# Optimization experiments

Measured on AMD Instinct MI355X. Metric: run time of the kernel, lower is better.

Reference implementation:

```python
import jax, jax.numpy as jnp
import numpy as np

T = 4096        # tokens
D = 1024        # input_dim
H = 2048        # expert_hidden_dim
O = 1024        # output_dim
E = 8           # num_experts
K = 2           # top_k


def setup_inputs() -> dict:
    key = jax.random.key(0)
    ks = jax.random.split(key, 7)
    s_in = 1.0 / np.sqrt(D)
    s_h = 1.0 / np.sqrt(H)
    return {
        "x": jax.random.normal(ks[0], (T, D), dtype=jnp.float32),
        "Wg": jax.random.uniform(ks[1], (D, E), jnp.float32, -s_in, s_in),
        "bg": jax.random.uniform(ks[2], (E,), jnp.float32, -s_in, s_in),
        "W1": jax.random.uniform(ks[3], (E, D, H), jnp.float32, -s_in, s_in),
        "b1": jax.random.uniform(ks[4], (E, H), jnp.float32, -s_in, s_in),
        "W2": jax.random.uniform(ks[5], (E, H, O), jnp.float32, -s_h, s_h),
        "b2": jax.random.uniform(ks[6], (E, O), jnp.float32, -s_h, s_h),
    }


def reference(x, Wg, bg, W1, b1, W2, b2):
    # Gating: top-k over expert logits, softmax over the k selected logits.
    logits = x @ Wg + bg                                  # [T, E]
    top_vals, top_idx = jax.lax.top_k(logits, K)          # [T, K]
    gates = jax.nn.softmax(top_vals, axis=-1)             # [T, K]

    # Expert MLPs (Linear -> ReLU -> Linear). Each token is processed by the
    # experts it routes to; since an expert's output on x is route-independent,
    # compute all expert outputs once and gather the selected ones (static
    # shapes, jit-friendly equivalent of the masked dispatch loop).
    h = jax.nn.relu(jnp.einsum('td,edh->eth', x, W1) + b1[:, None, :])  # [E,T,H]
    y = jnp.einsum('eth,eho->eto', h, W2) + b2[:, None, :]              # [E,T,O]

    sel = y[top_idx, jnp.arange(T)[:, None]]              # [T, K, O]
    # Weighted combine (scatter_add over batch_idx == per-token sum over K).
    return jnp.sum(sel * gates[..., None], axis=1)        # [T, O]
```

## Files before the change

### kernel.cpp

```cpp
#include <hip/hip_runtime.h>
#include <math.h>


#define T_TOK 4096
#define DIM   1024
#define HID   2048
#define OUTD  1024
#define NE    8

typedef __bf16 bf16_t;
typedef __bf16 bf16x8 __attribute__((ext_vector_type(8)));
typedef float  f32x4  __attribute__((ext_vector_type(4)));

typedef __attribute__((address_space(3))) void       as3_void;
typedef __attribute__((address_space(1))) const void as1_void;
#define GLDS16(src, dst) \
  __builtin_amdgcn_global_load_lds((as1_void*)(src), (as3_void*)(dst), 16, 0, 0)

#define FENCE() asm volatile("" ::: "memory")
#define BARRIER() do { FENCE(); __builtin_amdgcn_s_barrier(); FENCE(); } while (0)
#define LGKM_WAIT() do { \
    asm volatile("s_waitcnt lgkmcnt(0)" ::: "memory"); \
    __builtin_amdgcn_sched_barrier(0); } while (0)
#define VMW_RING() do { \
    if (wid < 4) asm volatile("s_waitcnt vmcnt(4)" ::: "memory"); \
    else         asm volatile("s_waitcnt vmcnt(3)" ::: "memory"); } while (0)
#define VM_WAIT0() asm volatile("s_waitcnt vmcnt(0)" ::: "memory")

__global__ void k_gate(const float* __restrict__ x, const float* __restrict__ Wg,
                       const float* __restrict__ bg, int* __restrict__ einfo,
                       float2* __restrict__ gpair, bf16_t* __restrict__ xb) {
  int wid  = threadIdx.x >> 6;
  int lane = threadIdx.x & 63;
  int t = blockIdx.x * 4 + wid;

  const float4* xr = (const float4*)(x + (size_t)t * DIM);
  float4 xv4[4];
  float sf[NE];
#pragma unroll
  for (int e = 0; e < NE; ++e) sf[e] = 0.f;

#pragma unroll
  for (int i = 0; i < 4; ++i) {
    int q = lane + 64 * i;
    float4 xv = xr[q];
    xv4[i] = xv;
    int d = q * 4;
#pragma unroll
    for (int c = 0; c < 4; ++c) {
      float xc = (&xv.x)[c];
      const float4* wr = (const float4*)(Wg + (size_t)(d + c) * NE);
      float4 w0 = wr[0], w1 = wr[1];
      sf[0] += xc * w0.x; sf[1] += xc * w0.y;
      sf[2] += xc * w0.z; sf[3] += xc * w0.w;
      sf[4] += xc * w1.x; sf[5] += xc * w1.y;
      sf[6] += xc * w1.z; sf[7] += xc * w1.w;
    }
  }

  ushort4* xbr = (ushort4*)(xb + (size_t)t * DIM);
#pragma unroll
  for (int i = 0; i < 4; ++i) {
    union { bf16_t b[4]; ushort4 u; } cv;
    cv.b[0] = (bf16_t)xv4[i].x; cv.b[1] = (bf16_t)xv4[i].y;
    cv.b[2] = (bf16_t)xv4[i].z; cv.b[3] = (bf16_t)xv4[i].w;
    xbr[lane + 64 * i] = cv.u;
  }

  double s[NE];
#pragma unroll
  for (int e = 0; e < NE; ++e) s[e] = (double)sf[e];
#pragma unroll
  for (int off = 32; off > 0; off >>= 1) {
#pragma unroll
    for (int e = 0; e < NE; ++e) s[e] += __shfl_xor(s[e], off);
  }

  if (lane == 0) {
    double v0 = -1e300, v1 = -1e300;
    int i0 = 0, i1 = 0;
#pragma unroll
    for (int e = 0; e < NE; ++e) {
      double v = s[e] + (double)bg[e];
      if (v > v0)      { v1 = v0; i1 = i0; v0 = v; i0 = e; }
      else if (v > v1) { v1 = v;  i1 = e; }
    }
    float ex = expf((float)(v1 - v0));
    float inv = 1.0f / (1.0f + ex);
    einfo[t] = i0 | (i1 << 8);
    gpair[t] = make_float2(inv, ex * inv);
  }
}

__global__ void k_bin(const int* __restrict__ einfo, const float2* __restrict__ gpair,
                      int* __restrict__ cnt, int* __restrict__ offs,
                      int* __restrict__ elist, float* __restrict__ egate,
                      int* __restrict__ tokrec) {
  __shared__ int scnt[NE];
  int w = threadIdx.x >> 6;
  int lane = threadIdx.x & 63;
  unsigned long long below = (lane == 0) ? 0ull : ((~0ull) >> (64 - lane));
  int base = 0;
  for (int c = 0; c < T_TOK / 64; ++c) {
    int t = c * 64 + lane;
    int ei = einfo[t];
    float2 g = gpair[t];
    int e0 = ei & 0xff, e1 = ei >> 8;
    bool m0 = (e0 == w);
    bool m  = m0 || (e1 == w);
    unsigned long long mask = __ballot(m);
    if (m) {
      int pos = base + (int)__popcll(mask & below);
      elist[w * T_TOK + pos] = t;
      egate[w * T_TOK + pos] = m0 ? g.x : g.y;
      tokrec[2 * t + (m0 ? 0 : 1)] = (w << 16) | pos;
    }
    base += (int)__popcll(mask);
  }
  if (lane == 0) scnt[w] = base;
  __syncthreads();
  if (threadIdx.x == 0) {
    int a = 0;
#pragma unroll
    for (int e = 0; e < NE; ++e) {
      cnt[e] = scnt[e];
      offs[e] = a;
      a += scnt[e];
    }
    offs[NE] = a;
  }
}

__global__ void k_tr(const float* __restrict__ W, bf16_t* __restrict__ Wt,
                     int R, int C) {
  __shared__ float tile[64][68];
  size_t ebase = (size_t)blockIdx.z * R * C;
  int c0 = blockIdx.x * 64, r0 = blockIdx.y * 64;
  int tid = threadIdx.x;
  int ty = tid >> 4, tx = tid & 15;
#pragma unroll
  for (int i = 0; i < 4; ++i) {
    int row = ty + i * 16;
    float4 v = *(const float4*)&W[ebase + (size_t)(r0 + row) * C + c0 + tx * 4];
    *(float4*)&tile[row][tx * 4] = v;
  }
  __syncthreads();
  int oc = tid >> 2, seg = tid & 3;
#pragma unroll
  for (int half = 0; half < 2; ++half) {
    union { bf16_t b[8]; uint4 u; } cv;
#pragma unroll
    for (int r = 0; r < 8; ++r)
      cv.b[r] = (bf16_t)tile[seg * 16 + half * 8 + r][oc];
    *(uint4*)&Wt[ebase + (size_t)(c0 + oc) * R + r0 + seg * 16 + half * 8] = cv.u;
  }
}

#define STAGE_A(TT, HH) do { \
    char* _d = smem + (((TT) & 1) * 24576) + ((HH) * 12288); \
    GLDS16(Abase + offA[HH][0] + (TT) * 128, _d + tid * 16); \
    if (tid < 256) GLDS16(Abase + offA[HH][1] + (TT) * 128, _d + (512 + tid) * 16); \
  } while (0)

#define STAGE_B(TT, HH) do { \
    char* _d = smem + 49152 + (((TT) & 1) * 32768) + ((HH) * 16384); \
    GLDS16(Bbase + offB[HH][0] + (TT) * 128, _d + tid * 16); \
    GLDS16(Bbase + offB[HH][1] + (TT) * 128, _d + (512 + tid) * 16); \
  } while (0)

#define MFMA_Q(AF, BF, AH, BH) \
    _Pragma("unroll") for (int i = 0; i < 3; ++i) \
      _Pragma("unroll") for (int j = 0; j < 2; ++j) \
        _Pragma("unroll") for (int kk = 0; kk < 2; ++kk) \
          acc[(AH) * 3 + i][(BH) * 2 + j] = \
            __builtin_amdgcn_mfma_f32_16x16x32_bf16(AF[i][kk], BF[j][kk], \
                acc[(AH) * 3 + i][(BH) * 2 + j], 0, 0, 0)

#define RD_AF(SL) \
    _Pragma("unroll") for (int i = 0; i < 3; ++i) \
      _Pragma("unroll") for (int kk = 0; kk < 2; ++kk) \
        af[i][kk] = *(const bf16x8*)((SL) + rdA[i][kk])

#define KTILE(TT, NTc) do { \
    const char* _a0 = smem + (((TT) & 1) * 24576); \
    const char* _a1 = smem + (((TT) & 1) * 24576) + 12288; \
    const char* _b0 = smem + 49152 + (((TT) & 1) * 32768); \
    const char* _b1 = smem + 49152 + (((TT) & 1) * 32768) + 16384; \
    bf16x8 af[3][2], bf0[2][2], bf1[2][2]; \
    RD_AF(_a0); \
    _Pragma("unroll") for (int j = 0; j < 2; ++j) \
      _Pragma("unroll") for (int kk = 0; kk < 2; ++kk) { \
        bf0[j][kk] = *(const bf16x8*)(_b0 + rdB[j][kk]); \
        bf1[j][kk] = *(const bf16x8*)(_b1 + rdB[j][kk]); \
      } \
    if ((TT) + 1 < (NTc)) { STAGE_A((TT) + 1, 1); STAGE_B((TT) + 1, 1); } \
    BARRIER(); LGKM_WAIT(); \
    __builtin_amdgcn_s_setprio(1); \
    MFMA_Q(af, bf0, 0, 0); MFMA_Q(af, bf1, 0, 1); \
    __builtin_amdgcn_s_setprio(0); BARRIER(); \
    RD_AF(_a1); \
    if ((TT) + 2 < (NTc)) { STAGE_A((TT) + 2, 0); STAGE_B((TT) + 2, 0); \
      VMW_RING(); } \
    else { VM_WAIT0(); } \
    BARRIER(); LGKM_WAIT(); \
    __builtin_amdgcn_s_setprio(1); \
    MFMA_Q(af, bf0, 1, 0); MFMA_Q(af, bf1, 1, 1); \
    __builtin_amdgcn_s_setprio(0); BARRIER(); \
  } while (0)

__launch_bounds__(512, 2)
__global__ void k_gemm1(const bf16_t* __restrict__ xb, const bf16_t* __restrict__ W1t,
                        const float* __restrict__ b1, const int* __restrict__ cnt,
                        const int* __restrict__ offs, const int* __restrict__ elist,
                        bf16_t* __restrict__ hbuf) {
  const int e = blockIdx.z;
  const int count = cnt[e];
  const int rt = blockIdx.y;
  if (rt * 192 >= count) return;
  const int nt = blockIdx.x;

  __shared__ __align__(16) char smem[114688];

  const int tid = threadIdx.x, lane = tid & 63, wid = tid >> 6;
  const int wm = wid >> 2, wn = wid & 3;
  const int fr = lane & 15, lh = lane >> 4;

  unsigned offA[2][2], offB[2][2];
#pragma unroll
  for (int j = 0; j < 2; ++j) {
    int q = j * 512 + tid;
    int r = q >> 3, sfg = (q & 7) ^ (r & 7);
#pragma unroll
    for (int h = 0; h < 2; ++h) {
      int gr = rt * 192 + h * 96 + r;
      if (gr > count - 1) gr = count - 1;
      int tok = elist[e * T_TOK + gr];
      offA[h][j] = (unsigned)((tok * DIM + sfg * 8) * 2);
      int brow = nt * 256 + h * 128 + r;
      offB[h][j] = (unsigned)(((e * HID + brow) * DIM + sfg * 8) * 2);
    }
  }
  unsigned rdA[3][2], rdB[2][2];
#pragma unroll
  for (int i = 0; i < 3; ++i) {
    int r = wm * 48 + i * 16 + fr;
#pragma unroll
    for (int kk = 0; kk < 2; ++kk)
      rdA[i][kk] = (unsigned)(r * 128 + (((kk * 4 + lh) ^ (r & 7)) * 16));
  }
#pragma unroll
  for (int j = 0; j < 2; ++j) {
    int r = wn * 32 + j * 16 + fr;
#pragma unroll
    for (int kk = 0; kk < 2; ++kk)
      rdB[j][kk] = (unsigned)(r * 128 + (((kk * 4 + lh) ^ (r & 7)) * 16));
  }

  const char* Abase = (const char*)xb;
  const char* Bbase = (const char*)W1t;

  f32x4 acc[6][4];
#pragma unroll
  for (int i = 0; i < 6; ++i)
#pragma unroll
    for (int j = 0; j < 4; ++j) acc[i][j] = (f32x4){0.f, 0.f, 0.f, 0.f};

  const int NT = DIM / 64;
  STAGE_A(0, 0); STAGE_B(0, 0); STAGE_A(0, 1); STAGE_B(0, 1);
  STAGE_A(1, 0); STAGE_B(1, 0);
  VMW_RING();
  BARRIER();

  for (int t = 0; t < NT; ++t) KTILE(t, NT);

  const int hbase = offs[e];
#pragma unroll
  for (int mi = 0; mi < 6; ++mi) {
#pragma unroll
    for (int rr = 0; rr < 4; ++rr) {
      int rowp = rt * 192 + (mi / 3) * 96 + wm * 48 + (mi % 3) * 16 + lh * 4 + rr;
      if (rowp < count) {
        size_t hrow = (size_t)(hbase + rowp) * HID;
#pragma unroll
        for (int nj = 0; nj < 4; ++nj) {
          int col = nt * 256 + (nj >> 1) * 128 + wn * 32 + (nj & 1) * 16 + fr;
          float v = acc[mi][nj][rr] + b1[e * HID + col];
          hbuf[hrow + col] = (bf16_t)(v > 0.f ? v : 0.f);
        }
      }
    }
  }
}

__launch_bounds__(512, 2)
__global__ void k_gemm2(const bf16_t* __restrict__ hbuf, const bf16_t* __restrict__ W2t,
                        const float* __restrict__ b2, const int* __restrict__ cnt,
                        const int* __restrict__ offs, const float* __restrict__ egate,
                        float* __restrict__ y) {
  const int e = blockIdx.z;
  const int count = cnt[e];
  const int rt = blockIdx.y;
  if (rt * 192 >= count) return;
  const int nt = blockIdx.x;

  __shared__ __align__(16) char smem[114688];

  const int tid = threadIdx.x, lane = tid & 63, wid = tid >> 6;
  const int wm = wid >> 2, wn = wid & 3;
  const int fr = lane & 15, lh = lane >> 4;
  const int hbase = offs[e];

  unsigned offA[2][2], offB[2][2];
#pragma unroll
  for (int j = 0; j < 2; ++j) {
    int q = j * 512 + tid;
    int r = q >> 3, sfg = (q & 7) ^ (r & 7);
#pragma unroll
    for (int h = 0; h < 2; ++h) {
      int gr = rt * 192 + h * 96 + r;
      if (gr > count - 1) gr = count - 1;
      offA[h][j] = (unsigned)(((hbase + gr) * HID + sfg * 8) * 2);
      int brow = nt * 256 + h * 128 + r;
      offB[h][j] = (unsigned)(((e * OUTD + brow) * HID + sfg * 8) * 2);
    }
  }
  unsigned rdA[3][2], rdB[2][2];
#pragma unroll
  for (int i = 0; i < 3; ++i) {
    int r = wm * 48 + i * 16 + fr;
#pragma unroll
    for (int kk = 0; kk < 2; ++kk)
      rdA[i][kk] = (unsigned)(r * 128 + (((kk * 4 + lh) ^ (r & 7)) * 16));
  }
#pragma unroll
  for (int j = 0; j < 2; ++j) {
    int r = wn * 32 + j * 16 + fr;
#pragma unroll
    for (int kk = 0; kk < 2; ++kk)
      rdB[j][kk] = (unsigned)(r * 128 + (((kk * 4 + lh) ^ (r & 7)) * 16));
  }

  const char* Abase = (const char*)hbuf;
  const char* Bbase = (const char*)W2t;

  f32x4 acc[6][4];
#pragma unroll
  for (int i = 0; i < 6; ++i)
#pragma unroll
    for (int j = 0; j < 4; ++j) acc[i][j] = (f32x4){0.f, 0.f, 0.f, 0.f};

  const int NT = HID / 64;
  STAGE_A(0, 0); STAGE_B(0, 0); STAGE_A(0, 1); STAGE_B(0, 1);
  STAGE_A(1, 0); STAGE_B(1, 0);
  VMW_RING();
  BARRIER();

  for (int t = 0; t < NT; ++t) KTILE(t, NT);

#pragma unroll
  for (int mi = 0; mi < 6; ++mi) {
#pragma unroll
    for (int rr = 0; rr < 4; ++rr) {
      int rowp = rt * 192 + (mi / 3) * 96 + wm * 48 + (mi % 3) * 16 + lh * 4 + rr;
      if (rowp < count) {
        float gate = egate[e * T_TOK + rowp];
        size_t yrow = (size_t)(hbase + rowp) * OUTD;
#pragma unroll
        for (int nj = 0; nj < 4; ++nj) {
          int col = nt * 256 + (nj >> 1) * 128 + wn * 32 + (nj & 1) * 16 + fr;
          y[yrow + col] = gate * (acc[mi][nj][rr] + b2[e * OUTD + col]);
        }
      }
    }
  }
}

__global__ void k_combine(const float* __restrict__ y, const int* __restrict__ offs,
                          const int* __restrict__ tokrec, float* __restrict__ out) {
  int t = blockIdx.x;
  int r0 = tokrec[2 * t], r1 = tokrec[2 * t + 1];
  int s0 = offs[r0 >> 16] + (r0 & 0xffff);
  int s1 = offs[r1 >> 16] + (r1 & 0xffff);
  const float4* ya = (const float4*)(y + (size_t)s0 * OUTD);
  const float4* yb = (const float4*)(y + (size_t)s1 * OUTD);
  float4* o = (float4*)(out + (size_t)t * OUTD);
  int i = threadIdx.x;
  float4 a = ya[i], b = yb[i];
  o[i] = make_float4(a.x + b.x, a.y + b.y, a.z + b.z, a.w + b.w);
}

extern "C" void kernel_launch(void* const* d_in, const int* in_sizes, int n_in,
                              void* d_out, int out_size, void* d_ws, size_t ws_size,
                              hipStream_t stream) {
  const float* x  = (const float*)d_in[0];
  const float* Wg = (const float*)d_in[1];
  const float* bg = (const float*)d_in[2];
  const float* W1 = (const float*)d_in[3];
  const float* b1 = (const float*)d_in[4];
  const float* W2 = (const float*)d_in[5];
  const float* b2 = (const float*)d_in[6];
  float* out = (float*)d_out;

  char* ws = (char*)d_ws;
  int*    cnt    = (int*)(ws);
  int*    offs   = (int*)(ws + 1024);
  int*    tokrec = (int*)(ws + 4096);
  int*    einfo  = (int*)(ws + 36864);
  float2* gpair  = (float2*)(ws + 53248);
  int*    elist  = (int*)(ws + 131072);
  float*  egate  = (float*)(ws + 262144);
  bf16_t* W1t    = (bf16_t*)(ws + (1u << 20));
  float*  y      = (float*)(ws + (1u << 20));
  bf16_t* W2t    = (bf16_t*)(ws + (1u << 20) + (32u << 20));
  bf16_t* xb     = (bf16_t*)(ws + (1u << 20) + (64u << 20));
  bf16_t* hbuf   = (bf16_t*)(ws + (1u << 20) + (72u << 20));

  k_gate<<<T_TOK / 4, 256, 0, stream>>>(x, Wg, bg, einfo, gpair, xb);
  k_bin<<<1, 512, 0, stream>>>(einfo, gpair, cnt, offs, elist, egate, tokrec);
  k_tr<<<dim3(HID / 64, DIM / 64, NE), 256, 0, stream>>>(W1, W1t, DIM, HID);
  k_tr<<<dim3(OUTD / 64, HID / 64, NE), 256, 0, stream>>>(W2, W2t, HID, OUTD);

  k_gemm1<<<dim3(HID / 256, 22, NE), 512, 0, stream>>>(
      xb, W1t, b1, cnt, offs, elist, hbuf);
  k_gemm2<<<dim3(OUTD / 256, 22, NE), 512, 0, stream>>>(
      hbuf, W2t, b2, cnt, offs, egate, y);
  k_combine<<<T_TOK, 256, 0, stream>>>(y, offs, tokrec, out);
}
```

Measured before the change: 208.9 us.

## Halve GEMM K-tile to 32 to cut LDS and raise occupancy

```diff
diff --git a/kernel.cpp b/kernel.cpp
--- a/kernel.cpp
+++ b/kernel.cpp
@@ -23,8 +23,8 @@
     asm volatile("s_waitcnt lgkmcnt(0)" ::: "memory"); \
     __builtin_amdgcn_sched_barrier(0); } while (0)
 #define VMW_RING() do { \
-    if (wid < 4) asm volatile("s_waitcnt vmcnt(4)" ::: "memory"); \
-    else         asm volatile("s_waitcnt vmcnt(3)" ::: "memory"); } while (0)
+    if (wid < 6) asm volatile("s_waitcnt vmcnt(2)" ::: "memory"); \
+    else         asm volatile("s_waitcnt vmcnt(1)" ::: "memory"); } while (0)
 #define VM_WAIT0() asm volatile("s_waitcnt vmcnt(0)" ::: "memory")
 
 __global__ void k_gate(const float* __restrict__ x, const float* __restrict__ Wg,
@@ -157,42 +157,37 @@
 }
 
 #define STAGE_A(TT, HH) do { \
-    char* _d = smem + (((TT) & 1) * 24576) + ((HH) * 12288); \
-    GLDS16(Abase + offA[HH][0] + (TT) * 128, _d + tid * 16); \
-    if (tid < 256) GLDS16(Abase + offA[HH][1] + (TT) * 128, _d + (512 + tid) * 16); \
-  } while (0)
+    if (tid < 384) { \
+      char* _d = smem + ((((TT) & 1) * 2 + (HH)) * 6144); \
+      GLDS16(Abase + offA[HH] + (TT) * 64, _d + tid * 16); \
+    } } while (0)
 
 #define STAGE_B(TT, HH) do { \
-    char* _d = smem + 49152 + (((TT) & 1) * 32768) + ((HH) * 16384); \
-    GLDS16(Bbase + offB[HH][0] + (TT) * 128, _d + tid * 16); \
-    GLDS16(Bbase + offB[HH][1] + (TT) * 128, _d + (512 + tid) * 16); \
-  } while (0)
+    char* _d = smem + 24576 + ((((TT) & 1) * 2 + (HH)) * 8192); \
+    GLDS16(Bbase + offB[HH] + (TT) * 64, _d + tid * 16); } while (0)
 
 #define MFMA_Q(AF, BF, AH, BH) \
     _Pragma("unroll") for (int i = 0; i < 3; ++i) \
       _Pragma("unroll") for (int j = 0; j < 2; ++j) \
-        _Pragma("unroll") for (int kk = 0; kk < 2; ++kk) \
-          acc[(AH) * 3 + i][(BH) * 2 + j] = \
-            __builtin_amdgcn_mfma_f32_16x16x32_bf16(AF[i][kk], BF[j][kk], \
-                acc[(AH) * 3 + i][(BH) * 2 + j], 0, 0, 0)
+        acc[(AH) * 3 + i][(BH) * 2 + j] = \
+          __builtin_amdgcn_mfma_f32_16x16x32_bf16(AF[i], BF[j], \
+              acc[(AH) * 3 + i][(BH) * 2 + j], 0, 0, 0)
 
 #define RD_AF(SL) \
     _Pragma("unroll") for (int i = 0; i < 3; ++i) \
-      _Pragma("unroll") for (int kk = 0; kk < 2; ++kk) \
-        af[i][kk] = *(const bf16x8*)((SL) + rdA[i][kk])
+        af[i] = *(const bf16x8*)((SL) + rdA[i])
 
 #define KTILE(TT, NTc) do { \
-    const char* _a0 = smem + (((TT) & 1) * 24576); \
-    const char* _a1 = smem + (((TT) & 1) * 24576) + 12288; \
-    const char* _b0 = smem + 49152 + (((TT) & 1) * 32768); \
-    const char* _b1 = smem + 49152 + (((TT) & 1) * 32768) + 16384; \
-    bf16x8 af[3][2], bf0[2][2], bf1[2][2]; \
+    const char* _a0 = smem + ((((TT) & 1) * 2 + 0) * 6144); \
+    const char* _a1 = smem + ((((TT) & 1) * 2 + 1) * 6144); \
+    const char* _b0 = smem + 24576 + ((((TT) & 1) * 2 + 0) * 8192); \
+    const char* _b1 = smem + 24576 + ((((TT) & 1) * 2 + 1) * 8192); \
+    bf16x8 af[3], bf0[2], bf1[2]; \
     RD_AF(_a0); \
-    _Pragma("unroll") for (int j = 0; j < 2; ++j) \
-      _Pragma("unroll") for (int kk = 0; kk < 2; ++kk) { \
-        bf0[j][kk] = *(const bf16x8*)(_b0 + rdB[j][kk]); \
-        bf1[j][kk] = *(const bf16x8*)(_b1 + rdB[j][kk]); \
-      } \
+    _Pragma("unroll") for (int j = 0; j < 2; ++j) { \
+      bf0[j] = *(const bf16x8*)(_b0 + rdB[j]); \
+      bf1[j] = *(const bf16x8*)(_b1 + rdB[j]); \
+    } \
     if ((TT) + 1 < (NTc)) { STAGE_A((TT) + 1, 1); STAGE_B((TT) + 1, 1); } \
     BARRIER(); LGKM_WAIT(); \
     __builtin_amdgcn_s_setprio(1); \
@@ -208,7 +203,7 @@
     __builtin_amdgcn_s_setprio(0); BARRIER(); \
   } while (0)
 
-__launch_bounds__(512, 2)
+__launch_bounds__(512, 4)
 __global__ void k_gemm1(const bf16_t* __restrict__ xb, const bf16_t* __restrict__ W1t,
                         const float* __restrict__ b1, const int* __restrict__ cnt,
                         const int* __restrict__ offs, const int* __restrict__ elist,
@@ -219,41 +214,36 @@
   if (rt * 192 >= count) return;
   const int nt = blockIdx.x;
 
-  __shared__ __align__(16) char smem[114688];
+  __shared__ __align__(16) char smem[57344];
 
   const int tid = threadIdx.x, lane = tid & 63, wid = tid >> 6;
   const int wm = wid >> 2, wn = wid & 3;
   const int fr = lane & 15, lh = lane >> 4;
 
-  unsigned offA[2][2], offB[2][2];
-#pragma unroll
-  for (int j = 0; j < 2; ++j) {
-    int q = j * 512 + tid;
-    int r = q >> 3, sfg = (q & 7) ^ (r & 7);
-#pragma unroll
-    for (int h = 0; h < 2; ++h) {
-      int gr = rt * 192 + h * 96 + r;
-      if (gr > count - 1) gr = count - 1;
-      int tok = elist[e * T_TOK + gr];
-      offA[h][j] = (unsigned)((tok * DIM + sfg * 8) * 2);
-      int brow = nt * 256 + h * 128 + r;
-      offB[h][j] = (unsigned)(((e * HID + brow) * DIM + sfg * 8) * 2);
-    }
-  }
-  unsigned rdA[3][2], rdB[2][2];
+  const int srow = tid >> 2;
+  const int sfg  = (tid & 3) ^ ((srow >> 1) & 3);
+  unsigned offA[2], offB[2];
+#pragma unroll
+  for (int h = 0; h < 2; ++h) {
+    int ar = srow < 96 ? srow : 95;
+    int gr = rt * 192 + h * 96 + ar;
+    if (gr > count - 1) gr = count - 1;
+    int tok = elist[e * T_TOK + gr];
+    offA[h] = (unsigned)((tok * DIM + sfg * 8) * 2);
+    int brow = nt * 256 + h * 128 + srow;
+    offB[h] = (unsigned)(((e * HID + brow) * DIM + sfg * 8) * 2);
+  }
+
+  unsigned rdA[3], rdB[2];
 #pragma unroll
   for (int i = 0; i < 3; ++i) {
     int r = wm * 48 + i * 16 + fr;
-#pragma unroll
-    for (int kk = 0; kk < 2; ++kk)
-      rdA[i][kk] = (unsigned)(r * 128 + (((kk * 4 + lh) ^ (r & 7)) * 16));
+    rdA[i] = (unsigned)(r * 64 + ((lh ^ ((r >> 1) & 3)) * 16));
   }
 #pragma unroll
   for (int j = 0; j < 2; ++j) {
     int r = wn * 32 + j * 16 + fr;
-#pragma unroll
-    for (int kk = 0; kk < 2; ++kk)
-      rdB[j][kk] = (unsigned)(r * 128 + (((kk * 4 + lh) ^ (r & 7)) * 16));
+    rdB[j] = (unsigned)(r * 64 + ((lh ^ ((r >> 1) & 3)) * 16));
   }
 
   const char* Abase = (const char*)xb;
@@ -265,7 +255,7 @@
 #pragma unroll
     for (int j = 0; j < 4; ++j) acc[i][j] = (f32x4){0.f, 0.f, 0.f, 0.f};
 
-  const int NT = DIM / 64;
+  const int NT = DIM / 32;
   STAGE_A(0, 0); STAGE_B(0, 0); STAGE_A(0, 1); STAGE_B(0, 1);
   STAGE_A(1, 0); STAGE_B(1, 0);
   VMW_RING();
@@ -292,7 +282,7 @@
   }
 }
 
-__launch_bounds__(512, 2)
+__launch_bounds__(512, 4)
 __global__ void k_gemm2(const bf16_t* __restrict__ hbuf, const bf16_t* __restrict__ W2t,
                         const float* __restrict__ b2, const int* __restrict__ cnt,
                         const int* __restrict__ offs, const float* __restrict__ egate,
@@ -303,41 +293,36 @@
   if (rt * 192 >= count) return;
   const int nt = blockIdx.x;
 
-  __shared__ __align__(16) char smem[114688];
+  __shared__ __align__(16) char smem[57344];
 
   const int tid = threadIdx.x, lane = tid & 63, wid = tid >> 6;
   const int wm = wid >> 2, wn = wid & 3;
   const int fr = lane & 15, lh = lane >> 4;
   const int hbase = offs[e];
 
-  unsigned offA[2][2], offB[2][2];
-#pragma unroll
-  for (int j = 0; j < 2; ++j) {
-    int q = j * 512 + tid;
-    int r = q >> 3, sfg = (q & 7) ^ (r & 7);
-#pragma unroll
-    for (int h = 0; h < 2; ++h) {
-      int gr = rt * 192 + h * 96 + r;
-      if (gr > count - 1) gr = count - 1;
-      offA[h][j] = (unsigned)(((hbase + gr) * HID + sfg * 8) * 2);
-      int brow = nt * 256 + h * 128 + r;
-      offB[h][j] = (unsigned)(((e * OUTD + brow) * HID + sfg * 8) * 2);
-    }
-  }
-  unsigned rdA[3][2], rdB[2][2];
+  const int srow = tid >> 2;
+  const int sfg  = (tid & 3) ^ ((srow >> 1) & 3);
+  unsigned offA[2], offB[2];
+#pragma unroll
+  for (int h = 0; h < 2; ++h) {
+    int ar = srow < 96 ? srow : 95;
+    int gr = rt * 192 + h * 96 + ar;
+    if (gr > count - 1) gr = count - 1;
+    offA[h] = (unsigned)(((hbase + gr) * HID + sfg * 8) * 2);
+    int brow = nt * 256 + h * 128 + srow;
+    offB[h] = (unsigned)(((e * OUTD + brow) * HID + sfg * 8) * 2);
+  }
+
+  unsigned rdA[3], rdB[2];
 #pragma unroll
   for (int i = 0; i < 3; ++i) {
     int r = wm * 48 + i * 16 + fr;
-#pragma unroll
-    for (int kk = 0; kk < 2; ++kk)
-      rdA[i][kk] = (unsigned)(r * 128 + (((kk * 4 + lh) ^ (r & 7)) * 16));
+    rdA[i] = (unsigned)(r * 64 + ((lh ^ ((r >> 1) & 3)) * 16));
   }
 #pragma unroll
   for (int j = 0; j < 2; ++j) {
     int r = wn * 32 + j * 16 + fr;
-#pragma unroll
-    for (int kk = 0; kk < 2; ++kk)
-      rdB[j][kk] = (unsigned)(r * 128 + (((kk * 4 + lh) ^ (r & 7)) * 16));
+    rdB[j] = (unsigned)(r * 64 + ((lh ^ ((r >> 1) & 3)) * 16));
   }
 
   const char* Abase = (const char*)hbuf;
@@ -349,7 +334,7 @@
 #pragma unroll
     for (int j = 0; j < 4; ++j) acc[i][j] = (f32x4){0.f, 0.f, 0.f, 0.f};
 
-  const int NT = HID / 64;
+  const int NT = HID / 32;
   STAGE_A(0, 0); STAGE_B(0, 0); STAGE_A(0, 1); STAGE_B(0, 1);
   STAGE_A(1, 0); STAGE_B(1, 0);
   VMW_RING();
```

New measurement: 396.3 us. 1.9x slower.
